# Kernel tuning notes

Measured on AMD Instinct MI355X. Metric: run time of the kernel, lower is better.

## Reference

```python
import jax, jax.numpy as jnp
import numpy as np
from jax import lax

N_CENTERS = 1024
RADIUS = 0.2
N_SAMPLES = 32
IN_DIM = 64
MLP_DIMS = [64, 64, 128]
BN_EPS = 1e-5


def setup_inputs() -> dict:
    key = jax.random.key(0)
    ks = jax.random.split(key, 2 + 3)
    B, N = 16, 4096
    inp = {
        "xyz": jax.random.normal(ks[0], (B, N, 3), jnp.float32),
        "features": jax.random.normal(ks[1], (B, N, IN_DIM), jnp.float32),
    }
    dims = [IN_DIM + 3] + MLP_DIMS
    for i in range(3):
        inp[f"w{i}"] = jax.random.normal(ks[2 + i], (dims[i + 1], dims[i]), jnp.float32) / np.sqrt(dims[i])
        inp[f"b{i}"] = jnp.zeros((dims[i + 1],), jnp.float32)
        inp[f"gamma{i}"] = jnp.ones((dims[i + 1],), jnp.float32)
        inp[f"beta{i}"] = jnp.zeros((dims[i + 1],), jnp.float32)
    return inp


def farthest_point_sampling(xyz, n_samples):
    # xyz: (B, N, 3). Deterministic start index 0 (torch uses randint seed).
    B, N, _ = xyz.shape
    batch = jnp.arange(B)

    def step(carry, _):
        dist, idx = carry
        ctr = xyz[batch, idx]                       # (B, 3)
        d = jnp.sum((xyz - ctr[:, None, :]) ** 2, -1)  # (B, N)
        dist = jnp.minimum(dist, d)
        nidx = jnp.argmax(dist, axis=1)
        return (dist, nidx), idx

    init = (jnp.full((B, N), jnp.inf, dtype=xyz.dtype), jnp.zeros((B,), jnp.int32))
    _, sel = lax.scan(step, init, None, length=n_samples)
    return sel.T  # (B, n_samples)


def ball_query(xyz, query, radius, n_samples):
    # full pairwise sq-dists (B, M, N), keep n_samples nearest, clamp outside radius
    dists = jnp.sum((query[:, :, None, :] - xyz[:, None, :, :]) ** 2, -1)
    sorted_idx = jnp.argsort(dists, axis=-1)[:, :, :n_samples]          # (B, M, S)
    d_sorted = jnp.take_along_axis(dists, sorted_idx, axis=-1)
    mask = d_sorted > radius ** 2
    return jnp.where(mask, sorted_idx[:, :, :1], sorted_idx)


def _bn_relu(x, gamma, beta):
    # x: (B, M, S, C); batch-norm in training mode over (B, M, S)
    mean = jnp.mean(x, axis=(0, 1, 2))
    var = jnp.var(x, axis=(0, 1, 2))
    xn = (x - mean) * lax.rsqrt(var + BN_EPS)
    return jax.nn.relu(xn * gamma + beta)


def reference(xyz, features, w0, b0, gamma0, beta0, w1, b1, gamma1, beta1, w2, b2, gamma2, beta2):
    B = xyz.shape[0]
    batch = jnp.arange(B)
    fps_idx = farthest_point_sampling(xyz, N_CENTERS)                    # (B, M)
    new_xyz = xyz[batch[:, None], fps_idx]                               # (B, M, 3)
    ball_idx = ball_query(xyz, new_xyz, RADIUS, N_SAMPLES)               # (B, M, S)

    grouped_xyz = xyz[batch[:, None, None], ball_idx] - new_xyz[:, :, None, :]   # (B, M, S, 3)
    grouped_feat = features[batch[:, None, None], ball_idx]                       # (B, M, S, C)
    x = jnp.concatenate([grouped_xyz, grouped_feat], axis=-1)            # (B, M, S, 3+C)

    for w, b, g, be in ((w0, b0, gamma0, beta0), (w1, b1, gamma1, beta1), (w2, b2, gamma2, beta2)):
        x = jnp.einsum('bmsc,dc->bmsd', x, w) + b                        # 1x1 conv
        x = _bn_relu(x, g, be)

    new_features = jnp.max(x, axis=2)                                    # (B, M, d_out)
    return (new_xyz, new_features)
```

## Files before the change

kernel.cpp:

```cpp
#include <hip/hip_runtime.h>

#define B_ 16
#define N_ 4096
#define M_ 1024
#define S_ 32
#define IN_ 64
#define C0IN 67
#define C0 64
#define C1 64
#define C2 128
#define NTOT (B_*M_*S_)
#define R2 0.04f
#define CAP 1024
#define NBUCK 16
#define BQ_G 32
#define MCEN 16

#define FPS_T 256
#define FPS_PTS 16

#define DPP_U64_MAX(k, ctrl) { \
    unsigned int _lo = (unsigned int)(k), _hi = (unsigned int)((k) >> 32); \
    unsigned int _olo = (unsigned int)__builtin_amdgcn_update_dpp((int)_lo, (int)_lo, ctrl, 0xF, 0xF, false); \
    unsigned int _ohi = (unsigned int)__builtin_amdgcn_update_dpp((int)_hi, (int)_hi, ctrl, 0xF, 0xF, false); \
    unsigned long long _o = ((unsigned long long)_ohi << 32) | _olo; \
    if (_o > (k)) (k) = _o; }

__global__ __launch_bounds__(FPS_T, 1) void fps_kernel(const float* __restrict__ xyz,
                                                       int* __restrict__ fps_idx,
                                                       float* __restrict__ out_xyz) {
#pragma clang fp contract(off)
    __shared__ float4 pxyz[N_];
    __shared__ int    sel[M_];
    __shared__ __align__(16) unsigned long long slotk[2][4];
    int b = blockIdx.x, t = threadIdx.x;
    const float* xb = xyz + (size_t)b * N_ * 3;
    float lx[FPS_PTS], ly[FPS_PTS], lz[FPS_PTS], dl[FPS_PTS];
#pragma unroll
    for (int j = 0; j < FPS_PTS; j++) {
        int i = (j << 8) + t;
        float x = xb[3*i], y = xb[3*i+1], z = xb[3*i+2];
        lx[j] = x; ly[j] = y; lz[j] = z;
        dl[j] = __builtin_inff();
        pxyz[i] = make_float4(x, y, z, 0.f);
    }
    __syncthreads();
    int wid = t >> 6, lane = t & 63;
    int cur = 0;
    float4 cc = pxyz[0];
    for (int k = 0; k < M_; k++) {
        float cx = cc.x, cy = cc.y, cz = cc.z;
        if (t == 0) sel[k] = cur;
#pragma unroll
        for (int j = 0; j < FPS_PTS; j++)
            asm volatile("" : "+v"(lx[j]), "+v"(ly[j]), "+v"(lz[j]));
        float bv = -1.0f; int bi = 0x7fffffff;
#pragma unroll
        for (int j = 0; j < FPS_PTS; j++) {
            float dx = lx[j] - cx, dy = ly[j] - cy, dz = lz[j] - cz;
            float t0 = dx*dx, t1 = dy*dy, t2 = dz*dz;
            float d = (t0 + t1) + t2;
            float od = dl[j];
            float nd = d < od ? d : od;
            dl[j] = nd;
            if (nd > bv) { bv = nd; bi = (j << 8) + t; }
        }
        unsigned long long key = ((unsigned long long)__float_as_uint(bv) << 32)
                               | (unsigned int)(~bi);
        DPP_U64_MAX(key, 0x111);
        DPP_U64_MAX(key, 0x112);
        DPP_U64_MAX(key, 0x114);
        DPP_U64_MAX(key, 0x118);
        DPP_U64_MAX(key, 0x142);
        DPP_U64_MAX(key, 0x143);
        int p = k & 1;
        if (lane == 63) slotk[p][wid] = key;
        __syncthreads();
        ulonglong2 s01 = *(const ulonglong2*)&slotk[p][0];
        ulonglong2 s23 = *(const ulonglong2*)&slotk[p][2];
        unsigned long long kk = s01.x;
        if (s01.y > kk) kk = s01.y;
        if (s23.x > kk) kk = s23.x;
        if (s23.y > kk) kk = s23.y;
        cur = (int)(~(unsigned int)kk);
        cc = pxyz[cur];
    }
    __syncthreads();
    for (int i = t; i < M_; i += FPS_T) {
        int ix = sel[i];
        float4 q = pxyz[ix];
        fps_idx[b*M_ + i] = ix;
        out_xyz[(b*M_ + i)*3 + 0] = q.x;
        out_xyz[(b*M_ + i)*3 + 1] = q.y;
        out_xyz[(b*M_ + i)*3 + 2] = q.z;
    }
}

__global__ __launch_bounds__(256) void ballq_kernel(const float* __restrict__ xyz,
                                                    const int* __restrict__ fps_idx,
                                                    int* __restrict__ ball_idx) {
#pragma clang fp contract(off)
    __shared__ float4 pts[N_];
    __shared__ float cd[CAP];
    __shared__ int   ci[CAP];
    __shared__ int   cnt;
    __shared__ float rv[4];
    __shared__ int   ri[4];
    __shared__ int   slots[33];
    int blk = blockIdx.x;
    int b = blk >> 5;
    int g = blk & 31;
    int t = threadIdx.x;
    const float* xb = xyz + (size_t)b * N_ * 3;
    for (int i = t; i < N_; i += 256)
        pts[i] = make_float4(xb[i*3+0], xb[i*3+1], xb[i*3+2], 0.f);
    __syncthreads();
    for (int mm = 0; mm < BQ_G; mm++) {
        int m = (g << 5) + mm;
        if (t == 0) cnt = 0;
        __syncthreads();
        float4 c4 = pts[fps_idx[b*M_ + m]];
        float cx = c4.x, cy = c4.y, cz = c4.z;
        float bv = 3.4e38f; int bi = 0x7fffffff;
        for (int i = t; i < N_; i += 256) {
            float4 p = pts[i];
            float dx = p.x - cx, dy = p.y - cy, dz = p.z - cz;
            float t0 = dx*dx, t1 = dy*dy, t2 = dz*dz;
            float d = (t0 + t1) + t2;
            if (d < bv || (d == bv && i < bi)) { bv = d; bi = i; }
            if (d <= R2) {
                int pp = atomicAdd(&cnt, 1);
                if (pp < CAP) { cd[pp] = d; ci[pp] = i; }
            }
        }
        for (int off = 32; off >= 1; off >>= 1) {
            float ov = __shfl_xor(bv, off, 64);
            int   oi = __shfl_xor(bi, off, 64);
            if (ov < bv || (ov == bv && oi < bi)) { bv = ov; bi = oi; }
        }
        int w = t >> 6;
        if ((t & 63) == 0) { rv[w] = bv; ri[w] = bi; }
        __syncthreads();
        int n = cnt < CAP ? cnt : CAP;
        for (int j = t; j < n; j += 256) {
            float dj = cd[j]; int ij = ci[j];
            int rank = 0;
            for (int k = 0; k < n; k++) {
                float dk = cd[k]; int ik = ci[k];
                rank += (dk < dj) || (dk == dj && ik < ij);
            }
            if (rank < S_) slots[rank] = ij;
        }
        if (t == 0) {
            float v = rv[0]; int ix = ri[0];
            for (int j = 1; j < 4; j++)
                if (rv[j] < v || (rv[j] == v && ri[j] < ix)) { v = rv[j]; ix = ri[j]; }
            slots[32] = ix;
        }
        __syncthreads();
        if (t < S_) {
            int nearest = (n > 0) ? slots[0] : slots[32];
            int ix = (t < n) ? slots[t] : nearest;
            ball_idx[(size_t)(b*M_ + m)*S_ + t] = ix;
        }
    }
}


__global__ __launch_bounds__(256) void mlpS1_kernel(
    const float* __restrict__ xyz, const float* __restrict__ feat,
    const int* __restrict__ fps_idx, const int* __restrict__ ball_idx,
    const float* __restrict__ w0, const float* __restrict__ b0,
    float* __restrict__ zbuf, float* __restrict__ stats) {
    __shared__ __align__(16) float xs[S_][72];
    __shared__ float rsum[64][9], rsq[64][9];
    __shared__ int idxs[S_];
    int blk0 = blockIdx.x * MCEN, t = threadIdx.x;
    int b = blk0 >> 10;
    const float* xb = xyz + (size_t)b * N_ * 3;
    int dp = t & 31, sg = t >> 5;
    int d0 = dp * 2;
    float wA[72], wB[72];
    {
        const float* wa = w0 + (size_t)d0 * C0IN;
        const float* wb = wa + C0IN;
        wA[0] = wa[0]; wA[1] = wa[1]; wA[2] = wa[2]; wA[3] = 0.f;
        wB[0] = wb[0]; wB[1] = wb[1]; wB[2] = wb[2]; wB[3] = 0.f;
#pragma unroll
        for (int c = 0; c < 64; c++) { wA[4 + c] = wa[3 + c]; wB[4 + c] = wb[3 + c]; }
#pragma unroll
        for (int c = 68; c < 72; c++) { wA[c] = 0.f; wB[c] = 0.f; }
    }
    float bi0 = b0[d0], bi1 = b0[d0+1];
    if (t < 32) { xs[t][3] = 0.f; }
    else if (t < 160) { int s = (t - 32) >> 2; xs[s][68 + ((t - 32) & 3)] = 0.f; }
    float ls0 = 0.f, lq0 = 0.f, ls1 = 0.f, lq1 = 0.f;
    for (int e = 0; e < MCEN; e++) {
        int blk = blk0 + e;
        int m = blk & (M_ - 1);
        int cidx = fps_idx[b*M_ + m];
        float cx = xb[cidx*3+0], cy = xb[cidx*3+1], cz = xb[cidx*3+2];
        if (t < S_) idxs[t] = ball_idx[(size_t)blk * S_ + t];
        __syncthreads();
#pragma unroll
        for (int ii = 0; ii < 2; ii++) {
            int i = t + ii * 256;
            int s = i >> 4, c4 = i & 15;
            int p = idxs[s];
            float4 v = *(const float4*)&feat[((size_t)b*N_ + p)*IN_ + 4*c4];
            *(float4*)&xs[s][4 + 4*c4] = v;
        }
        if (t < 96) {
            int s = t >> 2, comp = t & 3;
            if (comp < 3) {
                int p = idxs[s];
                float v = (comp == 0) ? xb[p*3+0] - cx
                        : (comp == 1) ? xb[p*3+1] - cy
                                      : xb[p*3+2] - cz;
                xs[s][comp] = v;
            }
        } else if (t < 224) {
            int tt = t - 96;
            int s = 24 + (tt >> 2), comp = tt & 3;
            if (comp < 3 && s < 32) {
                int p = idxs[s];
                float v = (comp == 0) ? xb[p*3+0] - cx
                        : (comp == 1) ? xb[p*3+1] - cy
                                      : xb[p*3+2] - cz;
                xs[s][comp] = v;
            }
        }
        __syncthreads();
        float acc0[4], acc1[4];
#pragma unroll
        for (int q = 0; q < 4; q++) { acc0[q] = bi0; acc1[q] = bi1; }
#pragma unroll
        for (int q = 0; q < 4; q++) {
            const float4* x4 = (const float4*)&xs[sg*4 + q][0];
#pragma unroll
            for (int c4 = 0; c4 < 18; c4++) {
                float4 v = x4[c4];
                acc0[q] += v.x * wA[4*c4+0]; acc1[q] += v.x * wB[4*c4+0];
                acc0[q] += v.y * wA[4*c4+1]; acc1[q] += v.y * wB[4*c4+1];
                acc0[q] += v.z * wA[4*c4+2]; acc1[q] += v.z * wB[4*c4+2];
                acc0[q] += v.w * wA[4*c4+3]; acc1[q] += v.w * wB[4*c4+3];
            }
        }
        float* zt = zbuf + (size_t)blk * 2048;
#pragma unroll
        for (int q = 0; q < 4; q++) {
            int s = sg*4 + q;
            *(float2*)&zt[s*64 + d0] = make_float2(acc0[q], acc1[q]);
            ls0 += acc0[q]; lq0 += acc0[q]*acc0[q];
            ls1 += acc1[q]; lq1 += acc1[q]*acc1[q];
        }
    }
    rsum[d0][sg] = ls0; rsq[d0][sg] = lq0;
    rsum[d0+1][sg] = ls1; rsq[d0+1][sg] = lq1;
    __syncthreads();
    if (t < 64) {
        float s = 0.f, s2 = 0.f;
#pragma unroll
        for (int j = 0; j < 8; j++) { s += rsum[t][j]; s2 += rsq[t][j]; }
        float* sb = stats + (size_t)(blockIdx.x & (NBUCK-1)) * 512;
        atomicAdd(&sb[t], s);
        atomicAdd(&sb[64 + t], s2);
    }
}

__global__ __launch_bounds__(256) void mlpS2_kernel(
    float* __restrict__ zbuf,
    const float* __restrict__ w1, const float* __restrict__ b1,
    const float* __restrict__ g0, const float* __restrict__ be0,
    float* __restrict__ stats) {
    __shared__ __align__(16) float y0s[S_][C0];
    __shared__ float rsum[64][9], rsq[64][9];
    __shared__ float lc[128];
    int blk0 = blockIdx.x * MCEN, t = threadIdx.x;
    const float inv_n = 1.0f / (float)NTOT;
    if (t < 64) {
        float s = 0.f, s2 = 0.f;
        for (int j = 0; j < NBUCK; j++) { s += stats[j*512 + t]; s2 += stats[j*512 + 64 + t]; }
        float mean = s * inv_n, var = s2 * inv_n - mean * mean;
        float a = g0[t] * (1.0f / sqrtf(var + 1e-5f));
        lc[t] = a; lc[64 + t] = be0[t] - mean * a;
    }
    int dc = t & 63;
    int dp = t & 31, sg = t >> 5;
    int d0 = dp * 2;
    float wA[64], wB[64];
    {
        const float4* wa4 = (const float4*)(w1 + (size_t)d0 * C0);
        const float4* wb4 = (const float4*)(w1 + (size_t)(d0+1) * C0);
#pragma unroll
        for (int c4 = 0; c4 < 16; c4++) {
            float4 a = wa4[c4], bb = wb4[c4];
            wA[4*c4+0] = a.x;  wA[4*c4+1] = a.y;  wA[4*c4+2] = a.z;  wA[4*c4+3] = a.w;
            wB[4*c4+0] = bb.x; wB[4*c4+1] = bb.y; wB[4*c4+2] = bb.z; wB[4*c4+3] = bb.w;
        }
    }
    float bi0 = b1[d0], bi1 = b1[d0+1];
    __syncthreads();
    float a0c = lc[dc], c0c = lc[64 + dc];
    float ls0 = 0.f, lq0 = 0.f, ls1 = 0.f, lq1 = 0.f;
    for (int e = 0; e < MCEN; e++) {
        int blk = blk0 + e;
        float* zt = zbuf + (size_t)blk * 2048;
        float zv[8];
#pragma unroll
        for (int j = 0; j < 8; j++) zv[j] = zt[t + 256*j];
        if (e) __syncthreads();
#pragma unroll
        for (int j = 0; j < 8; j++) {
            float v = zv[j] * a0c + c0c;
            y0s[(t >> 6) + 4*j][dc] = v > 0.f ? v : 0.f;
        }
        __syncthreads();
        float acc0[4], acc1[4];
#pragma unroll
        for (int q = 0; q < 4; q++) { acc0[q] = bi0; acc1[q] = bi1; }
#pragma unroll
        for (int q = 0; q < 4; q++) {
            const float4* x4 = (const float4*)&y0s[sg*4 + q][0];
#pragma unroll
            for (int c4 = 0; c4 < 16; c4++) {
                float4 v = x4[c4];
                acc0[q] += v.x * wA[4*c4+0]; acc1[q] += v.x * wB[4*c4+0];
                acc0[q] += v.y * wA[4*c4+1]; acc1[q] += v.y * wB[4*c4+1];
                acc0[q] += v.z * wA[4*c4+2]; acc1[q] += v.z * wB[4*c4+2];
                acc0[q] += v.w * wA[4*c4+3]; acc1[q] += v.w * wB[4*c4+3];
            }
        }
#pragma unroll
        for (int q = 0; q < 4; q++) {
            int s = sg*4 + q;
            *(float2*)&zt[s*64 + d0] = make_float2(acc0[q], acc1[q]);
            ls0 += acc0[q]; lq0 += acc0[q]*acc0[q];
            ls1 += acc1[q]; lq1 += acc1[q]*acc1[q];
        }
    }
    rsum[d0][sg] = ls0; rsq[d0][sg] = lq0;
    rsum[d0+1][sg] = ls1; rsq[d0+1][sg] = lq1;
    __syncthreads();
    if (t < 64) {
        float s = 0.f, s2 = 0.f;
#pragma unroll
        for (int j = 0; j < 8; j++) { s += rsum[t][j]; s2 += rsq[t][j]; }
        float* sb = stats + (size_t)(blockIdx.x & (NBUCK-1)) * 512;
        atomicAdd(&sb[128 + t], s);
        atomicAdd(&sb[192 + t], s2);
    }
}

template<int STOREZ>
__global__ __launch_bounds__(256) void mlpS3_kernel(
    const float* __restrict__ zbuf,
    const float* __restrict__ w2, const float* __restrict__ b2,
    const float* __restrict__ g1, const float* __restrict__ be1,
    float* __restrict__ z2buf, float* __restrict__ stats) {
    __shared__ __align__(16) float y1s[S_][C1];
    __shared__ float rsum[128][5], rsq[128][5];
    __shared__ float lc[128];
    int blk0 = blockIdx.x * MCEN, t = threadIdx.x;
    const float inv_n = 1.0f / (float)NTOT;
    if (t < 64) {
        float s = 0.f, s2 = 0.f;
        for (int j = 0; j < NBUCK; j++) { s += stats[j*512 + 128 + t]; s2 += stats[j*512 + 192 + t]; }
        float mean = s * inv_n, var = s2 * inv_n - mean * mean;
        float a = g1[t] * (1.0f / sqrtf(var + 1e-5f));
        lc[t] = a; lc[64 + t] = be1[t] - mean * a;
    }
    int dc = t & 63;
    int dp = t & 63, sg = t >> 6;
    int d0 = dp * 2;
    float wA[64], wB[64];
    {
        const float4* wa4 = (const float4*)(w2 + (size_t)d0 * C1);
        const float4* wb4 = (const float4*)(w2 + (size_t)(d0+1) * C1);
#pragma unroll
        for (int c4 = 0; c4 < 16; c4++) {
            float4 a = wa4[c4], bb = wb4[c4];
            wA[4*c4+0] = a.x;  wA[4*c4+1] = a.y;  wA[4*c4+2] = a.z;  wA[4*c4+3] = a.w;
            wB[4*c4+0] = bb.x; wB[4*c4+1] = bb.y; wB[4*c4+2] = bb.z; wB[4*c4+3] = bb.w;
        }
    }
    float bi0 = b2[d0], bi1 = b2[d0+1];
    __syncthreads();
    float a1c = lc[dc], c1c = lc[64 + dc];
    float ls0 = 0.f, lq0 = 0.f, ls1 = 0.f, lq1 = 0.f;
    for (int e = 0; e < MCEN; e++) {
        int blk = blk0 + e;
        const float* zt = zbuf + (size_t)blk * 2048;
        float zv[8];
#pragma unroll
        for (int j = 0; j < 8; j++) zv[j] = zt[t + 256*j];
        if (e) __syncthreads();
#pragma unroll
        for (int j = 0; j < 8; j++) {
            float v = zv[j] * a1c + c1c;
            y1s[(t >> 6) + 4*j][dc] = v > 0.f ? v : 0.f;
        }
        __syncthreads();
        float acc0[8], acc1[8];
#pragma unroll
        for (int q = 0; q < 8; q++) { acc0[q] = bi0; acc1[q] = bi1; }
#pragma unroll
        for (int q = 0; q < 8; q++) {
            const float4* x4 = (const float4*)&y1s[sg*8 + q][0];
#pragma unroll
            for (int c4 = 0; c4 < 16; c4++) {
                float4 v = x4[c4];
                acc0[q] += v.x * wA[4*c4+0]; acc1[q] += v.x * wB[4*c4+0];
                acc0[q] += v.y * wA[4*c4+1]; acc1[q] += v.y * wB[4*c4+1];
                acc0[q] += v.z * wA[4*c4+2]; acc1[q] += v.z * wB[4*c4+2];
                acc0[q] += v.w * wA[4*c4+3]; acc1[q] += v.w * wB[4*c4+3];
            }
        }
        float* z2t = z2buf + (size_t)blk * 4096;
#pragma unroll
        for (int q = 0; q < 8; q++) {
            if (STOREZ) {
                int s = sg*8 + q;
                *(float2*)&z2t[s*128 + d0] = make_float2(acc0[q], acc1[q]);
            }
            ls0 += acc0[q]; lq0 += acc0[q]*acc0[q];
            ls1 += acc1[q]; lq1 += acc1[q]*acc1[q];
        }
    }
    rsum[d0][sg] = ls0; rsq[d0][sg] = lq0;
    rsum[d0+1][sg] = ls1; rsq[d0+1][sg] = lq1;
    __syncthreads();
    if (t < 128) {
        float s = 0.f, s2 = 0.f;
#pragma unroll
        for (int j = 0; j < 4; j++) { s += rsum[t][j]; s2 += rsq[t][j]; }
        float* sb = stats + (size_t)(blockIdx.x & (NBUCK-1)) * 512;
        atomicAdd(&sb[256 + t], s);
        atomicAdd(&sb[384 + t], s2);
    }
}

__global__ __launch_bounds__(256) void mlpS4z_kernel(
    const float* __restrict__ z2buf,
    const float* __restrict__ g2, const float* __restrict__ be2,
    const float* __restrict__ stats, float* __restrict__ out_feat) {
    __shared__ float red[256];
    __shared__ float lc[256];
    int blk = blockIdx.x, t = threadIdx.x;
    const float inv_n = 1.0f / (float)NTOT;
    if (t < 128) {
        float s = 0.f, s2 = 0.f;
        for (int j = 0; j < NBUCK; j++) { s += stats[j*512 + 256 + t]; s2 += stats[j*512 + 384 + t]; }
        float mean = s * inv_n, var = s2 * inv_n - mean * mean;
        float a = g2[t] * (1.0f / sqrtf(var + 1e-5f));
        lc[t] = a; lc[128 + t] = be2[t] - mean * a;
    }
    const float* z2t = z2buf + (size_t)blk * 4096;
    float zv[16];
#pragma unroll
    for (int j = 0; j < 16; j++) zv[j] = z2t[t + 256*j];
    __syncthreads();
    int d = t & 127;
    float a2 = lc[d], c2 = lc[128 + d];
    float lmax = -3.4e38f;
#pragma unroll
    for (int j = 0; j < 16; j++) {
        float v = zv[j] * a2 + c2;
        v = v > 0.f ? v : 0.f;
        lmax = v > lmax ? v : lmax;
    }
    red[t] = lmax;
    __syncthreads();
    if (t < 128) {
        float v = red[t] > red[t+128] ? red[t] : red[t+128];
        out_feat[(size_t)blk * C2 + t] = v;
    }
}

__global__ __launch_bounds__(256) void mlpS4r_kernel(
    const float* __restrict__ zbuf,
    const float* __restrict__ w2, const float* __restrict__ b2,
    const float* __restrict__ g1, const float* __restrict__ be1,
    const float* __restrict__ g2, const float* __restrict__ be2,
    const float* __restrict__ stats, float* __restrict__ out_feat) {
    __shared__ __align__(16) float y1s[S_][C1];
    __shared__ float rmax[128][5];
    __shared__ float lc[384];
    int blk0 = blockIdx.x * MCEN, t = threadIdx.x;
    const float inv_n = 1.0f / (float)NTOT;
    if (t < 64) {
        float s = 0.f, s2 = 0.f;
        for (int j = 0; j < NBUCK; j++) { s += stats[j*512 + 128 + t]; s2 += stats[j*512 + 192 + t]; }
        float mean = s * inv_n, var = s2 * inv_n - mean * mean;
        float a = g1[t] * (1.0f / sqrtf(var + 1e-5f));
        lc[t] = a; lc[64 + t] = be1[t] - mean * a;
    }
    if (t < 128) {
        float s = 0.f, s2 = 0.f;
        for (int j = 0; j < NBUCK; j++) { s += stats[j*512 + 256 + t]; s2 += stats[j*512 + 384 + t]; }
        float mean = s * inv_n, var = s2 * inv_n - mean * mean;
        float a = g2[t] * (1.0f / sqrtf(var + 1e-5f));
        lc[128 + t] = a; lc[256 + t] = be2[t] - mean * a;
    }
    int dc = t & 63;
    int dp = t & 63, sg = t >> 6;
    int d0 = dp * 2;
    float wA[64], wB[64];
    {
        const float4* wa4 = (const float4*)(w2 + (size_t)d0 * C1);
        const float4* wb4 = (const float4*)(w2 + (size_t)(d0+1) * C1);
#pragma unroll
        for (int c4 = 0; c4 < 16; c4++) {
            float4 a = wa4[c4], bb = wb4[c4];
            wA[4*c4+0] = a.x;  wA[4*c4+1] = a.y;  wA[4*c4+2] = a.z;  wA[4*c4+3] = a.w;
            wB[4*c4+0] = bb.x; wB[4*c4+1] = bb.y; wB[4*c4+2] = bb.z; wB[4*c4+3] = bb.w;
        }
    }
    float bi0 = b2[d0], bi1 = b2[d0+1];
    __syncthreads();
    float a1c = lc[dc], c1c = lc[64 + dc];
    float a20 = lc[128 + d0], c20 = lc[256 + d0];
    float a21 = lc[128 + d0 + 1], c21 = lc[256 + d0 + 1];
    for (int e = 0; e < MCEN; e++) {
        int blk = blk0 + e;
        const float* zt = zbuf + (size_t)blk * 2048;
        float zv[8];
#pragma unroll
        for (int j = 0; j < 8; j++) zv[j] = zt[t + 256*j];
        if (e) __syncthreads();
#pragma unroll
        for (int j = 0; j < 8; j++) {
            float v = zv[j] * a1c + c1c;
            y1s[(t >> 6) + 4*j][dc] = v > 0.f ? v : 0.f;
        }
        __syncthreads();
        float acc0[8], acc1[8];
#pragma unroll
        for (int q = 0; q < 8; q++) { acc0[q] = bi0; acc1[q] = bi1; }
#pragma unroll
        for (int q = 0; q < 8; q++) {
            const float4* x4 = (const float4*)&y1s[sg*8 + q][0];
#pragma unroll
            for (int c4 = 0; c4 < 16; c4++) {
                float4 v = x4[c4];
                acc0[q] += v.x * wA[4*c4+0]; acc1[q] += v.x * wB[4*c4+0];
                acc0[q] += v.y * wA[4*c4+1]; acc1[q] += v.y * wB[4*c4+1];
                acc0[q] += v.z * wA[4*c4+2]; acc1[q] += v.z * wB[4*c4+2];
                acc0[q] += v.w * wA[4*c4+3]; acc1[q] += v.w * wB[4*c4+3];
            }
        }
        float lm0 = -3.4e38f, lm1 = -3.4e38f;
#pragma unroll
        for (int q = 0; q < 8; q++) {
            float v0 = acc0[q] * a20 + c20; v0 = v0 > 0.f ? v0 : 0.f;
            float v1 = acc1[q] * a21 + c21; v1 = v1 > 0.f ? v1 : 0.f;
            lm0 = v0 > lm0 ? v0 : lm0;
            lm1 = v1 > lm1 ? v1 : lm1;
        }
        rmax[d0][sg] = lm0; rmax[d0+1][sg] = lm1;
        __syncthreads();
        if (t < 128) {
            float v = rmax[t][0];
#pragma unroll
            for (int j = 1; j < 4; j++) v = rmax[t][j] > v ? rmax[t][j] : v;
            out_feat[(size_t)blk * C2 + t] = v;
        }
    }
}

extern "C" void kernel_launch(void* const* d_in, const int* in_sizes, int n_in,
                              void* d_out, int out_size, void* d_ws, size_t ws_size,
                              hipStream_t stream) {
    const float* xyz  = (const float*)d_in[0];
    const float* feat = (const float*)d_in[1];
    const float* w0 = (const float*)d_in[2];  const float* b0 = (const float*)d_in[3];
    const float* g0 = (const float*)d_in[4];  const float* be0 = (const float*)d_in[5];
    const float* w1 = (const float*)d_in[6];  const float* b1 = (const float*)d_in[7];
    const float* g1 = (const float*)d_in[8];  const float* be1 = (const float*)d_in[9];
    const float* w2 = (const float*)d_in[10]; const float* b2 = (const float*)d_in[11];
    const float* g2 = (const float*)d_in[12]; const float* be2 = (const float*)d_in[13];
    float* out_xyz  = (float*)d_out;
    float* out_feat = out_xyz + B_*M_*3;

    int* fps_i  = (int*)d_ws;
    int* ball_i = (int*)((char*)d_ws + 65536);
    float* stats = (float*)((char*)d_ws + 65536 + 2097152);
    size_t zoff = 65536 + 2097152 + (size_t)NBUCK*512*4;
    float* zbuf = (float*)((char*)d_ws + zoff);
    float* z2buf = zbuf + (size_t)B_*M_ * 2048;
    size_t need2 = zoff + (size_t)B_*M_ * 2048 * 4 + (size_t)B_*M_ * 4096 * 4;
    bool stage_z2 = ws_size >= need2;

    hipMemsetAsync(stats, 0, NBUCK*512*sizeof(float), stream);
    fps_kernel<<<B_, FPS_T, 0, stream>>>(xyz, fps_i, out_xyz);
    ballq_kernel<<<B_ * (M_/BQ_G), 256, 0, stream>>>(xyz, fps_i, ball_i);
    mlpS1_kernel<<<(B_*M_)/MCEN, 256, 0, stream>>>(xyz, feat, fps_i, ball_i, w0, b0, zbuf, stats);
    mlpS2_kernel<<<(B_*M_)/MCEN, 256, 0, stream>>>(zbuf, w1, b1, g0, be0, stats);
    if (stage_z2) {
        mlpS3_kernel<1><<<(B_*M_)/MCEN, 256, 0, stream>>>(zbuf, w2, b2, g1, be1, z2buf, stats);
        mlpS4z_kernel<<<B_*M_, 256, 0, stream>>>(z2buf, g2, be2, stats, out_feat);
    } else {
        mlpS3_kernel<0><<<(B_*M_)/MCEN, 256, 0, stream>>>(zbuf, w2, b2, g1, be1, z2buf, stats);
        mlpS4r_kernel<<<(B_*M_)/MCEN, 256, 0, stream>>>(zbuf, w2, b2, g1, be1, g2, be2, stats, out_feat);
    }
}
```

Before: 1.461 ms.

## Store per-centre max/min of layer-3 output instead of full activations

The third conv stage now reduces each centre's 32 samples to a per-channel max and min. The final kernel selects one of them based on the sign of the batch-norm scale, then applies BN and ReLU, so the large intermediate activation tensor is no longer written and re-read. The BN-input loads and shared stores in the MLP stages are also vectorised to float4. This costs an extra block synchronisation per centre in the layer-3 kernel.

New measurement: 1.488 ms. About the same (+1.8%).

```diff
diff --git a/kernel.cpp b/kernel.cpp
--- a/kernel.cpp
+++ b/kernel.cpp
@@ -275,7 +275,7 @@
     float* __restrict__ stats) {
     __shared__ __align__(16) float y0s[S_][C0];
     __shared__ float rsum[64][9], rsq[64][9];
-    __shared__ float lc[128];
+    __shared__ __align__(16) float lc[128];
     int blk0 = blockIdx.x * MCEN, t = threadIdx.x;
     const float inv_n = 1.0f / (float)NTOT;
     if (t < 64) {
@@ -285,7 +285,7 @@
         float a = g0[t] * (1.0f / sqrtf(var + 1e-5f));
         lc[t] = a; lc[64 + t] = be0[t] - mean * a;
     }
-    int dc = t & 63;
+    int dv = (4*t) & 63;
     int dp = t & 31, sg = t >> 5;
     int d0 = dp * 2;
     float wA[64], wB[64];
@@ -301,19 +301,28 @@
     }
     float bi0 = b1[d0], bi1 = b1[d0+1];
     __syncthreads();
-    float a0c = lc[dc], c0c = lc[64 + dc];
+    float4 av = *(const float4*)&lc[dv];
+    float4 cv = *(const float4*)&lc[64 + dv];
     float ls0 = 0.f, lq0 = 0.f, ls1 = 0.f, lq1 = 0.f;
     for (int e = 0; e < MCEN; e++) {
         int blk = blk0 + e;
         float* zt = zbuf + (size_t)blk * 2048;
-        float zv[8];
-#pragma unroll
-        for (int j = 0; j < 8; j++) zv[j] = zt[t + 256*j];
+        float4 zv0 = *(const float4*)&zt[4*t];
+        float4 zv1 = *(const float4*)&zt[4*t + 1024];
         if (e) __syncthreads();
-#pragma unroll
-        for (int j = 0; j < 8; j++) {
-            float v = zv[j] * a0c + c0c;
-            y0s[(t >> 6) + 4*j][dc] = v > 0.f ? v : 0.f;
+        {
+            int s0 = (4*t) >> 6, s1 = s0 + 16;
+            float4 y0, y1;
+            y0.x = zv0.x*av.x + cv.x; y0.y = zv0.y*av.y + cv.y;
+            y0.z = zv0.z*av.z + cv.z; y0.w = zv0.w*av.w + cv.w;
+            y1.x = zv1.x*av.x + cv.x; y1.y = zv1.y*av.y + cv.y;
+            y1.z = zv1.z*av.z + cv.z; y1.w = zv1.w*av.w + cv.w;
+            y0.x = y0.x > 0.f ? y0.x : 0.f; y0.y = y0.y > 0.f ? y0.y : 0.f;
+            y0.z = y0.z > 0.f ? y0.z : 0.f; y0.w = y0.w > 0.f ? y0.w : 0.f;
+            y1.x = y1.x > 0.f ? y1.x : 0.f; y1.y = y1.y > 0.f ? y1.y : 0.f;
+            y1.z = y1.z > 0.f ? y1.z : 0.f; y1.w = y1.w > 0.f ? y1.w : 0.f;
+            *(float4*)&y0s[s0][dv] = y0;
+            *(float4*)&y0s[s1][dv] = y1;
         }
         __syncthreads();
         float acc0[4], acc1[4];
@@ -352,15 +361,16 @@
     }
 }
 
-template<int STOREZ>
+template<int STOREMM>
 __global__ __launch_bounds__(256) void mlpS3_kernel(
     const float* __restrict__ zbuf,
     const float* __restrict__ w2, const float* __restrict__ b2,
     const float* __restrict__ g1, const float* __restrict__ be1,
-    float* __restrict__ z2buf, float* __restrict__ stats) {
+    float* __restrict__ mmbuf, float* __restrict__ stats) {
     __shared__ __align__(16) float y1s[S_][C1];
     __shared__ float rsum[128][5], rsq[128][5];
-    __shared__ float lc[128];
+    __shared__ float rmx[128][5], rmn[128][5];
+    __shared__ __align__(16) float lc[128];
     int blk0 = blockIdx.x * MCEN, t = threadIdx.x;
     const float inv_n = 1.0f / (float)NTOT;
     if (t < 64) {
@@ -370,7 +380,7 @@
         float a = g1[t] * (1.0f / sqrtf(var + 1e-5f));
         lc[t] = a; lc[64 + t] = be1[t] - mean * a;
     }
-    int dc = t & 63;
+    int dv = (4*t) & 63;
     int dp = t & 63, sg = t >> 6;
     int d0 = dp * 2;
     float wA[64], wB[64];
@@ -386,19 +396,28 @@
     }
     float bi0 = b2[d0], bi1 = b2[d0+1];
     __syncthreads();
-    float a1c = lc[dc], c1c = lc[64 + dc];
+    float4 av = *(const float4*)&lc[dv];
+    float4 cv = *(const float4*)&lc[64 + dv];
     float ls0 = 0.f, lq0 = 0.f, ls1 = 0.f, lq1 = 0.f;
     for (int e = 0; e < MCEN; e++) {
         int blk = blk0 + e;
         const float* zt = zbuf + (size_t)blk * 2048;
-        float zv[8];
-#pragma unroll
-        for (int j = 0; j < 8; j++) zv[j] = zt[t + 256*j];
+        float4 zv0 = *(const float4*)&zt[4*t];
+        float4 zv1 = *(const float4*)&zt[4*t + 1024];
         if (e) __syncthreads();
-#pragma unroll
-        for (int j = 0; j < 8; j++) {
-            float v = zv[j] * a1c + c1c;
-            y1s[(t >> 6) + 4*j][dc] = v > 0.f ? v : 0.f;
+        {
+            int s0 = (4*t) >> 6, s1 = s0 + 16;
+            float4 y0, y1;
+            y0.x = zv0.x*av.x + cv.x; y0.y = zv0.y*av.y + cv.y;
+            y0.z = zv0.z*av.z + cv.z; y0.w = zv0.w*av.w + cv.w;
+            y1.x = zv1.x*av.x + cv.x; y1.y = zv1.y*av.y + cv.y;
+            y1.z = zv1.z*av.z + cv.z; y1.w = zv1.w*av.w + cv.w;
+            y0.x = y0.x > 0.f ? y0.x : 0.f; y0.y = y0.y > 0.f ? y0.y : 0.f;
+            y0.z = y0.z > 0.f ? y0.z : 0.f; y0.w = y0.w > 0.f ? y0.w : 0.f;
+            y1.x = y1.x > 0.f ? y1.x : 0.f; y1.y = y1.y > 0.f ? y1.y : 0.f;
+            y1.z = y1.z > 0.f ? y1.z : 0.f; y1.w = y1.w > 0.f ? y1.w : 0.f;
+            *(float4*)&y1s[s0][dv] = y0;
+            *(float4*)&y1s[s1][dv] = y1;
         }
         __syncthreads();
         float acc0[8], acc1[8];
@@ -416,15 +435,31 @@
                 acc0[q] += v.w * wA[4*c4+3]; acc1[q] += v.w * wB[4*c4+3];
             }
         }
-        float* z2t = z2buf + (size_t)blk * 4096;
 #pragma unroll
         for (int q = 0; q < 8; q++) {
-            if (STOREZ) {
-                int s = sg*8 + q;
-                *(float2*)&z2t[s*128 + d0] = make_float2(acc0[q], acc1[q]);
-            }
             ls0 += acc0[q]; lq0 += acc0[q]*acc0[q];
             ls1 += acc1[q]; lq1 += acc1[q]*acc1[q];
+        }
+        if (STOREMM) {
+            float m0 = acc0[0], n0 = acc0[0], m1 = acc1[0], n1 = acc1[0];
+#pragma unroll
+            for (int q = 1; q < 8; q++) {
+                m0 = acc0[q] > m0 ? acc0[q] : m0;  n0 = acc0[q] < n0 ? acc0[q] : n0;
+                m1 = acc1[q] > m1 ? acc1[q] : m1;  n1 = acc1[q] < n1 ? acc1[q] : n1;
+            }
+            rmx[d0][sg] = m0; rmn[d0][sg] = n0;
+            rmx[d0+1][sg] = m1; rmn[d0+1][sg] = n1;
+            __syncthreads();
+            if (t < 128) {
+                float mx = rmx[t][0], mn = rmn[t][0];
+#pragma unroll
+                for (int j = 1; j < 4; j++) {
+                    mx = rmx[t][j] > mx ? rmx[t][j] : mx;
+                    mn = rmn[t][j] < mn ? rmn[t][j] : mn;
+                }
+                mmbuf[(size_t)blk * 256 + t] = mx;
+                mmbuf[(size_t)blk * 256 + 128 + t] = mn;
+            }
         }
     }
     rsum[d0][sg] = ls0; rsq[d0][sg] = lq0;
@@ -440,11 +475,10 @@
     }
 }
 
-__global__ __launch_bounds__(256) void mlpS4z_kernel(
-    const float* __restrict__ z2buf,
+__global__ __launch_bounds__(256) void mlpS4m_kernel(
+    const float* __restrict__ mmbuf,
     const float* __restrict__ g2, const float* __restrict__ be2,
     const float* __restrict__ stats, float* __restrict__ out_feat) {
-    __shared__ float red[256];
     __shared__ float lc[256];
     int blk = blockIdx.x, t = threadIdx.x;
     const float inv_n = 1.0f / (float)NTOT;
@@ -455,25 +489,15 @@
         float a = g2[t] * (1.0f / sqrtf(var + 1e-5f));
         lc[t] = a; lc[128 + t] = be2[t] - mean * a;
     }
-    const float* z2t = z2buf + (size_t)blk * 4096;
-    float zv[16];
-#pragma unroll
-    for (int j = 0; j < 16; j++) zv[j] = z2t[t + 256*j];
-    __syncthreads();
-    int d = t & 127;
-    float a2 = lc[d], c2 = lc[128 + d];
-    float lmax = -3.4e38f;
-#pragma unroll
-    for (int j = 0; j < 16; j++) {
-        float v = zv[j] * a2 + c2;
-        v = v > 0.f ? v : 0.f;
-        lmax = v > lmax ? v : lmax;
-    }
-    red[t] = lmax;
-    __syncthreads();
-    if (t < 128) {
-        float v = red[t] > red[t+128] ? red[t] : red[t+128];
-        out_feat[(size_t)blk * C2 + t] = v;
+    __syncthreads();
+    size_t base = (size_t)blk * 4096;
+    for (int i = t; i < 4096; i += 256) {
+        size_t gi = base + i;
+        int cen = (int)(gi >> 7), d = (int)(gi & 127);
+        float a = lc[d], c = lc[128 + d];
+        float z = (a > 0.f) ? mmbuf[(size_t)cen*256 + d] : mmbuf[(size_t)cen*256 + 128 + d];
+        float v = a * z + c;
+        out_feat[gi] = v > 0.f ? v : 0.f;
     }
 }
 
@@ -485,7 +509,7 @@
     const float* __restrict__ stats, float* __restrict__ out_feat) {
     __shared__ __align__(16) float y1s[S_][C1];
     __shared__ float rmax[128][5];
-    __shared__ float lc[384];
+    __shared__ __align__(16) float lc[384];
     int blk0 = blockIdx.x * MCEN, t = threadIdx.x;
     const float inv_n = 1.0f / (float)NTOT;
     if (t < 64) {
@@ -502,7 +526,7 @@
         float a = g2[t] * (1.0f / sqrtf(var + 1e-5f));
         lc[128 + t] = a; lc[256 + t] = be2[t] - mean * a;
     }
-    int dc = t & 63;
+    int dv = (4*t) & 63;
     int dp = t & 63, sg = t >> 6;
     int d0 = dp * 2;
     float wA[64], wB[64];
@@ -518,20 +542,29 @@
     }
     float bi0 = b2[d0], bi1 = b2[d0+1];
     __syncthreads();
-    float a1c = lc[dc], c1c = lc[64 + dc];
+    float4 av = *(const float4*)&lc[dv];
+    float4 cvv = *(const float4*)&lc[64 + dv];
     float a20 = lc[128 + d0], c20 = lc[256 + d0];
     float a21 = lc[128 + d0 + 1], c21 = lc[256 + d0 + 1];
     for (int e = 0; e < MCEN; e++) {
         int blk = blk0 + e;
         const float* zt = zbuf + (size_t)blk * 2048;
-        float zv[8];
-#pragma unroll
-        for (int j = 0; j < 8; j++) zv[j] = zt[t + 256*j];
+        float4 zv0 = *(const float4*)&zt[4*t];
+        float4 zv1 = *(const float4*)&zt[4*t + 1024];
         if (e) __syncthreads();
-#pragma unroll
-        for (int j = 0; j < 8; j++) {
-            float v = zv[j] * a1c + c1c;
-            y1s[(t >> 6) + 4*j][dc] = v > 0.f ? v : 0.f;
+        {
+            int s0 = (4*t) >> 6, s1 = s0 + 16;
+            float4 y0, y1;
+            y0.x = zv0.x*av.x + cvv.x; y0.y = zv0.y*av.y + cvv.y;
+            y0.z = zv0.z*av.z + cvv.z; y0.w = zv0.w*av.w + cvv.w;
+            y1.x = zv1.x*av.x + cvv.x; y1.y = zv1.y*av.y + cvv.y;
+            y1.z = zv1.z*av.z + cvv.z; y1.w = zv1.w*av.w + cvv.w;
+            y0.x = y0.x > 0.f ? y0.x : 0.f; y0.y = y0.y > 0.f ? y0.y : 0.f;
+            y0.z = y0.z > 0.f ? y0.z : 0.f; y0.w = y0.w > 0.f ? y0.w : 0.f;
+            y1.x = y1.x > 0.f ? y1.x : 0.f; y1.y = y1.y > 0.f ? y1.y : 0.f;
+            y1.z = y1.z > 0.f ? y1.z : 0.f; y1.w = y1.w > 0.f ? y1.w : 0.f;
+            *(float4*)&y1s[s0][dv] = y0;
+            *(float4*)&y1s[s1][dv] = y1;
         }
         __syncthreads();
         float acc0[8], acc1[8];
@@ -587,20 +620,20 @@
     float* stats = (float*)((char*)d_ws + 65536 + 2097152);
     size_t zoff = 65536 + 2097152 + (size_t)NBUCK*512*4;
     float* zbuf = (float*)((char*)d_ws + zoff);
-    float* z2buf = zbuf + (size_t)B_*M_ * 2048;
-    size_t need2 = zoff + (size_t)B_*M_ * 2048 * 4 + (size_t)B_*M_ * 4096 * 4;
-    bool stage_z2 = ws_size >= need2;
+    float* mmbuf = zbuf + (size_t)B_*M_ * 2048;
+    size_t need_mm = zoff + (size_t)B_*M_ * 2048 * 4 + (size_t)B_*M_ * 256 * 4;
+    bool have_mm = ws_size >= need_mm;
 
     hipMemsetAsync(stats, 0, NBUCK*512*sizeof(float), stream);
     fps_kernel<<<B_, FPS_T, 0, stream>>>(xyz, fps_i, out_xyz);
     ballq_kernel<<<B_ * (M_/BQ_G), 256, 0, stream>>>(xyz, fps_i, ball_i);
     mlpS1_kernel<<<(B_*M_)/MCEN, 256, 0, stream>>>(xyz, feat, fps_i, ball_i, w0, b0, zbuf, stats);
     mlpS2_kernel<<<(B_*M_)/MCEN, 256, 0, stream>>>(zbuf, w1, b1, g0, be0, stats);
-    if (stage_z2) {
-        mlpS3_kernel<1><<<(B_*M_)/MCEN, 256, 0, stream>>>(zbuf, w2, b2, g1, be1, z2buf, stats);
-        mlpS4z_kernel<<<B_*M_, 256, 0, stream>>>(z2buf, g2, be2, stats, out_feat);
+    if (have_mm) {
+        mlpS3_kernel<1><<<(B_*M_)/MCEN, 256, 0, stream>>>(zbuf, w2, b2, g1, be1, mmbuf, stats);
+        mlpS4m_kernel<<<512, 256, 0, stream>>>(mmbuf, g2, be2, stats, out_feat);
     } else {
-        mlpS3_kernel<0><<<(B_*M_)/MCEN, 256, 0, stream>>>(zbuf, w2, b2, g1, be1, z2buf, stats);
+        mlpS3_kernel<0><<<(B_*M_)/MCEN, 256, 0, stream>>>(zbuf, w2, b2, g1, be1, mmbuf, stats);
         mlpS4r_kernel<<<(B_*M_)/MCEN, 256, 0, stream>>>(zbuf, w2, b2, g1, be1, g2, be2, stats, out_feat);
     }
 }
```
